# Optimization experiments

Measured on AMD Instinct MI355X. Metric: run time of the kernel, lower is better.

The kernel has to match this reference:

```python
import jax, jax.numpy as jnp
import numpy as np

B, T, E = 64, 64, 256
S, ENC = 128, 1024
RNN, ATT, DENSE = 1024, 1024, 8000


def setup_inputs() -> dict:
    key = jax.random.key(0)
    ks = jax.random.split(key, 16)
    s = 0.02
    return {
        "initial_input": jax.random.normal(ks[0], (B, T, E), jnp.float32),
        "hidden": jax.random.normal(ks[1], (B, RNN), jnp.float32),
        "cell": jax.random.normal(ks[2], (B, RNN), jnp.float32),
        "encoder_output": jax.random.normal(ks[3], (B, S, ENC), jnp.float32),
        "W1": jax.random.normal(ks[4], (RNN, ATT), jnp.float32) * s,
        "b1": jnp.zeros((ATT,), jnp.float32),
        "W2": jax.random.normal(ks[5], (ENC, ATT), jnp.float32) * s,
        "b2": jnp.zeros((ATT,), jnp.float32),
        "V": jax.random.normal(ks[6], (ATT, 1), jnp.float32) * s,
        "bV": jnp.zeros((1,), jnp.float32),
        "kernel": jax.random.normal(ks[7], (ENC + E, 4 * RNN), jnp.float32) * s,
        "rkernel": jax.random.normal(ks[8], (RNN, 4 * RNN), jnp.float32) * s,
        "bias": jnp.zeros((4 * RNN,), jnp.float32),
        "Wd": jax.random.normal(ks[9], (RNN, DENSE), jnp.float32) * s,
        "bd": jnp.zeros((DENSE,), jnp.float32),
        "seq_len": T,
    }


def _decode(initial_input, hidden, cell, encoder_output,
            W1, b1, W2, b2, V, bV, kernel, rkernel, bias, Wd, bd):
    # Keys W2(encoder_output) are step-independent: precompute once. [B,S,ATT]
    keys = jnp.einsum('bse,ea->bsa', encoder_output, W2) + b2

    def step(carry, x_t):
        h, c = carry
        # Bahdanau attention: score = V^T tanh(W1 h + W2 enc)
        q = h @ W1 + b1                                  # [B,ATT]
        score = jnp.tanh(q[:, None, :] + keys) @ V + bV   # [B,S,1]
        attn = jax.nn.softmax(score, axis=1)              # [B,S,1]
        ctx = jnp.sum(attn * encoder_output, axis=1)      # [B,ENC]
        # LSTM cell (Keras gate order i,f,g,o; sigmoid/tanh activations)
        inp = jnp.concatenate([ctx, x_t], axis=-1)        # [B,ENC+E]
        z = inp @ kernel + h @ rkernel + bias              # [B,4*RNN]
        i, f, g, o = jnp.split(z, 4, axis=-1)
        i = jax.nn.sigmoid(i)
        f = jax.nn.sigmoid(f)
        g = jnp.tanh(g)
        o = jax.nn.sigmoid(o)
        c_new = f * c + i * g
        h_new = o * jnp.tanh(c_new)
        logits = h_new @ Wd + bd                           # [B,DENSE]
        return (h_new, c_new), logits

    xs = jnp.swapaxes(initial_input, 0, 1)  # [T,B,E]
    (h, c), logits = jax.lax.scan(step, (hidden, cell), xs)
    outputs = jnp.swapaxes(logits, 0, 1)    # [B,T,DENSE]
    return outputs, h, c


def reference(initial_input, hidden, cell, encoder_output,
              W1, b1, W2, b2, V, bV, kernel, rkernel, bias, Wd, bd, seq_len):
    # seq_len == initial_input.shape[1] (static); the Python loop in the
    # original is expressed as an efficient lax.scan over decode steps.
    return _decode(initial_input[:, :seq_len, :], hidden, cell, encoder_output,
                   W1, b1, W2, b2, V, bV, kernel, rkernel, bias, Wd, bd)
```

## Files before the change

kernel.cpp:

```cpp
#include <hip/hip_runtime.h>
#include <hip/hip_bf16.h>
#include <stdint.h>


typedef __attribute__((ext_vector_type(8))) short short8;
typedef __attribute__((ext_vector_type(4))) float floatx4;
typedef __attribute__((ext_vector_type(4))) unsigned short ushortx4;

__device__ __forceinline__ float b2f(unsigned short u) {
    union { unsigned int i; float f; } v; v.i = ((unsigned int)u) << 16; return v.f;
}
__device__ __forceinline__ unsigned short f2b(float f) {
    union { float f; unsigned int i; } v; v.f = f;
    unsigned int r = v.i + 0x7fffu + ((v.i >> 16) & 1u);
    return (unsigned short)(r >> 16);
}
__device__ __forceinline__ float ftanh(float x) {
    x = fminf(15.f, fmaxf(-15.f, x));
    float e = __expf(2.f * x);
    return (e - 1.f) * __builtin_amdgcn_rcpf(e + 1.f);
}
__device__ __forceinline__ float vtanh(float x) {
    return __builtin_fmaf(-2.f, __builtin_amdgcn_rcpf(__expf(2.f * x) + 1.f), 1.f);
}
__device__ __forceinline__ float fsig(float x) {
    return __builtin_amdgcn_rcpf(1.f + __expf(-x));
}
__device__ __forceinline__ void ld_lds16(const void* g, void* l) {
    __builtin_amdgcn_global_load_lds((const __attribute__((address_space(1))) void*)g,
                                     (__attribute__((address_space(3))) void*)l, 16, 0, 0);
}

__device__ __forceinline__ void tr_tile(
    float (*tile)[33], const float* __restrict__ src, int srcld,
    unsigned short* __restrict__ dst, int dstld, int coloff, int perm,
    int bx, int by, int tid)
{
    const int k0 = by * 32, n0 = bx * 32;
    const int r = tid >> 3, c = (tid & 7) * 4;
    int n = n0 + c;
    int cn = perm ? ((((n >> 4) & 3) << 10) | ((n >> 6) << 4) | (n & 15)) : n;
    float4 v = *(const float4*)&src[(size_t)(k0 + r) * srcld + cn];
    tile[r][c + 0] = v.x; tile[r][c + 1] = v.y;
    tile[r][c + 2] = v.z; tile[r][c + 3] = v.w;
    __syncthreads();
    const int nr = tid >> 3, kc = (tid & 7) * 4;
    ushortx4 o;
    o[0] = f2b(tile[kc + 0][nr]);
    o[1] = f2b(tile[kc + 1][nr]);
    o[2] = f2b(tile[kc + 2][nr]);
    o[3] = f2b(tile[kc + 3][nr]);
    *(ushortx4*)&dst[(size_t)(n0 + nr) * dstld + coloff + k0 + kc] = o;
}

__global__ __launch_bounds__(256) void prep_all(
    const float* __restrict__ W2, unsigned short* __restrict__ W2T,
    const float* __restrict__ W1, unsigned short* __restrict__ W1T,
    const float* __restrict__ Wk, const float* __restrict__ rk,
    unsigned short* __restrict__ KRT,
    const float* __restrict__ Wd, unsigned short* __restrict__ WdT,
    const float* __restrict__ enc, unsigned short* __restrict__ enc_bf,
    const float* __restrict__ hidden, const float* __restrict__ cell,
    float* __restrict__ cb, unsigned short* __restrict__ hbf)
{
    __shared__ float tile[32][33];
    const int lid = blockIdx.x, tid = threadIdx.x;
    if (lid < 1024) {
        tr_tile(tile, W2, 1024, W2T, 1024, 0, 0, lid & 31, lid >> 5, tid);
    } else if (lid < 2048) {
        int l = lid - 1024;
        tr_tile(tile, W1, 1024, W1T, 1024, 0, 0, l & 31, l >> 5, tid);
    } else if (lid < 6144) {
        int l = lid - 2048;
        tr_tile(tile, Wk, 4096, KRT, 2304, 0, 1, l & 127, l >> 7, tid);
    } else if (lid < 7168) {
        int l = lid - 6144;
        tr_tile(tile, Wk + 1024 * 4096, 4096, KRT, 2304, 1024, 1, l & 127, l >> 7, tid);
    } else if (lid < 11264) {
        int l = lid - 7168;
        tr_tile(tile, rk, 4096, KRT, 2304, 1280, 1, l & 127, l >> 7, tid);
    } else if (lid < 19264) {
        int l = lid - 11264;
        tr_tile(tile, Wd, 8000, WdT, 1024, 0, 0, l % 250, l / 250, tid);
    } else if (lid < 27456) {
        int i = (lid - 19264) * 256 + tid;
        float4 v = ((const float4*)enc)[i];
        ushortx4 o;
        o[0] = f2b(v.x); o[1] = f2b(v.y); o[2] = f2b(v.z); o[3] = f2b(v.w);
        ((ushortx4*)enc_bf)[i] = o;
    } else {
        int idx = (lid - 27456) * 256 + tid;
        float h = hidden[idx], c = cell[idx];
        cb[idx] = c; hbf[idx] = f2b(h);
    }
}

__global__ __launch_bounds__(256) void gemm_bf16_128(
    const unsigned short* __restrict__ A, int lda,
    const unsigned short* __restrict__ BT, int ldbt, int K,
    float* __restrict__ Cf, unsigned short* __restrict__ Cb,
    int ldc, int ncols, const float* __restrict__ bias, int swz)
{
    __shared__ __align__(16) unsigned short As[128 * 32];
    __shared__ __align__(16) unsigned short Bs[128 * 32];
    const int tid = threadIdx.x, wave = tid >> 6, lane = tid & 63;
    const int q = lane >> 4, lm = lane & 15;
    const int wr = wave >> 1, wc = wave & 1;
    int bx = blockIdx.x, by = blockIdx.y;
    if (swz) {
        int bid = by * gridDim.x + bx;
        int xcd = bid & 7, l = bid >> 3;
        bx = xcd * 8 + (l & 7);
        by = l >> 3;
    }
    const int m0 = by * 128, n0 = bx * 128;
    const int srow = lane >> 2;
    const int gch = (lane & 3) ^ ((lane >> 3) & 3);
    const unsigned short* Ag0 = A + (size_t)(m0 + wave * 32 + srow) * lda + gch * 8;
    const unsigned short* Ag1 = Ag0 + (size_t)16 * lda;
    const unsigned short* Bg0 = BT + (size_t)(n0 + wave * 32 + srow) * ldbt + gch * 8;
    const unsigned short* Bg1 = Bg0 + (size_t)16 * ldbt;
    unsigned short* Al0 = &As[(wave * 32) * 32];
    unsigned short* Al1 = &As[(wave * 32 + 16) * 32];
    unsigned short* Bl0 = &Bs[(wave * 32) * 32];
    unsigned short* Bl1 = &Bs[(wave * 32 + 16) * 32];

    const floatx4 z4 = {0.f, 0.f, 0.f, 0.f};
    floatx4 acc[4][4];
#pragma unroll
    for (int i = 0; i < 4; i++)
#pragma unroll
        for (int j = 0; j < 4; j++) acc[i][j] = z4;
    const int ach = ((q ^ ((lm >> 1) & 3))) * 8;

    for (int kb = 0; kb < K; kb += 32) {
        ld_lds16(Ag0 + kb, Al0);
        ld_lds16(Ag1 + kb, Al1);
        ld_lds16(Bg0 + kb, Bl0);
        ld_lds16(Bg1 + kb, Bl1);
        __syncthreads();
        short8 a[4], b[4];
#pragma unroll
        for (int i = 0; i < 4; i++) a[i] = *(const short8*)&As[(wr * 64 + i * 16 + lm) * 32 + ach];
#pragma unroll
        for (int j = 0; j < 4; j++) b[j] = *(const short8*)&Bs[(wc * 64 + j * 16 + lm) * 32 + ach];
#pragma unroll
        for (int i = 0; i < 4; i++)
#pragma unroll
            for (int j = 0; j < 4; j++)
                acc[i][j] = __builtin_amdgcn_mfma_f32_16x16x32_bf16(a[i], b[j], acc[i][j], 0, 0, 0);
        __syncthreads();
    }
    const int rb = m0 + wr * 64 + q * 4;
#pragma unroll
    for (int i = 0; i < 4; i++) {
#pragma unroll
        for (int j = 0; j < 4; j++) {
            int col = n0 + wc * 64 + j * 16 + lm;
            if (col < ncols) {
                float bv = bias ? bias[col] : 0.f;
#pragma unroll
                for (int r = 0; r < 4; r++) {
                    float v = acc[i][j][r] + bv;
                    size_t idx = (size_t)(rb + i * 16 + r) * ldc + col;
                    if (Cf) Cf[idx] = v;
                    if (Cb) Cb[idx] = f2b(v);
                }
            }
        }
    }
}

__global__ __launch_bounds__(256) void gemm64_split(
    const unsigned short* __restrict__ A, int lda,
    const unsigned short* __restrict__ BT, int ldbt,
    int kchunk, float* __restrict__ Cpart, int ldc)
{
    __shared__ __align__(16) unsigned short As[4][64 * 32];
    __shared__ __align__(16) unsigned short Bs[4][64 * 32];
    const int tid = threadIdx.x, wave = tid >> 6, lane = tid & 63;
    const int q = lane >> 4, lm = lane & 15;
    const int n0 = blockIdx.x * 64;
    const int k0 = blockIdx.z * kchunk;
    const int srow = lane >> 2;
    const int gch = (lane & 3) ^ ((lane >> 3) & 3);
    const unsigned short* Ag = A + (size_t)(wave * 16 + srow) * lda + k0 + gch * 8;
    const unsigned short* Bg = BT + (size_t)(n0 + wave * 16 + srow) * ldbt + k0 + gch * 8;
    const int loff = (wave * 16) * 32;
    const floatx4 z4 = {0.f, 0.f, 0.f, 0.f};
    floatx4 acc0 = z4, acc1 = z4, acc2 = z4, acc3 = z4;
    const int ach = ((q ^ ((lm >> 1) & 3))) * 8;
    const int nit = kchunk >> 5;

#pragma unroll
    for (int p = 0; p < 3; ++p) {
        if (p < nit) {
            ld_lds16(Ag + p * 32, &As[p][loff]);
            ld_lds16(Bg + p * 32, &Bs[p][loff]);
        }
    }
    for (int it = 0; it < nit; ++it) {
        const int st = it & 3;
        if (it + 2 < nit)      asm volatile("s_waitcnt vmcnt(4)\n\ts_barrier" ::: "memory");
        else if (it + 1 < nit) asm volatile("s_waitcnt vmcnt(2)\n\ts_barrier" ::: "memory");
        else                   asm volatile("s_waitcnt vmcnt(0)\n\ts_barrier" ::: "memory");
        if (it + 3 < nit) {
            const int sn = (it + 3) & 3;
            ld_lds16(Ag + (it + 3) * 32, &As[sn][loff]);
            ld_lds16(Bg + (it + 3) * 32, &Bs[sn][loff]);
        }
        short8 a  = *(const short8*)&As[st][(wave * 16 + lm) * 32 + ach];
        short8 b0 = *(const short8*)&Bs[st][(0 * 16 + lm) * 32 + ach];
        short8 b1 = *(const short8*)&Bs[st][(1 * 16 + lm) * 32 + ach];
        short8 b2 = *(const short8*)&Bs[st][(2 * 16 + lm) * 32 + ach];
        short8 b3 = *(const short8*)&Bs[st][(3 * 16 + lm) * 32 + ach];
        acc0 = __builtin_amdgcn_mfma_f32_16x16x32_bf16(a, b0, acc0, 0, 0, 0);
        acc1 = __builtin_amdgcn_mfma_f32_16x16x32_bf16(a, b1, acc1, 0, 0, 0);
        acc2 = __builtin_amdgcn_mfma_f32_16x16x32_bf16(a, b2, acc2, 0, 0, 0);
        acc3 = __builtin_amdgcn_mfma_f32_16x16x32_bf16(a, b3, acc3, 0, 0, 0);
    }
    float* Cp = Cpart + (size_t)blockIdx.z * 64 * ldc;
    const int rb = wave * 16 + q * 4;
    floatx4 accs[4] = {acc0, acc1, acc2, acc3};
#pragma unroll
    for (int i = 0; i < 4; i++) {
        int col = n0 + i * 16 + lm;
#pragma unroll
        for (int r = 0; r < 4; r++) Cp[(size_t)(rb + r) * ldc + col] = accs[i][r];
    }
}

__global__ __launch_bounds__(256) void attn_scores(
    const float* __restrict__ qp, const float* __restrict__ b1,
    const unsigned short* __restrict__ keys,
    const float* __restrict__ V, const float* __restrict__ bV,
    float* __restrict__ sc)
{
    __shared__ float qs[1024];
    __shared__ float vs[1024];
    const int b = blockIdx.y, sg = blockIdx.x;
    const int tid = threadIdx.x, wave = tid >> 6, lane = tid & 63;
    {
        float4 a0 = ((const float4*)(qp + (size_t)b * 1024))[tid];
        float4 a1 = ((const float4*)(qp + 65536 + (size_t)b * 1024))[tid];
        float4 a2 = ((const float4*)(qp + 131072 + (size_t)b * 1024))[tid];
        float4 a3 = ((const float4*)(qp + 196608 + (size_t)b * 1024))[tid];
        float4 ab = ((const float4*)b1)[tid];
        float4 av = ((const float4*)V)[tid];
        float4 r;
        r.x = a0.x + a1.x + a2.x + a3.x + ab.x;
        r.y = a0.y + a1.y + a2.y + a3.y + ab.y;
        r.z = a0.z + a1.z + a2.z + a3.z + ab.z;
        r.w = a0.w + a1.w + a2.w + a3.w + ab.w;
        *(float4*)&qs[tid * 4] = r;
        *(float4*)&vs[tid * 4] = av;
    }
    __syncthreads();
    float qr[16], vr[16];
#pragma unroll
    for (int i = 0; i < 4; i++) {
        float4 tq = *(const float4*)&qs[lane * 16 + i * 4];
        float4 tv = *(const float4*)&vs[lane * 16 + i * 4];
        qr[i * 4 + 0] = tq.x; qr[i * 4 + 1] = tq.y; qr[i * 4 + 2] = tq.z; qr[i * 4 + 3] = tq.w;
        vr[i * 4 + 0] = tv.x; vr[i * 4 + 1] = tv.y; vr[i * 4 + 2] = tv.z; vr[i * 4 + 3] = tv.w;
    }
    const float bv0 = bV[0];
#pragma unroll
    for (int i = 0; i < 4; i++) {
        const int s = sg * 16 + wave * 4 + i;
        const uint4* kp = (const uint4*)(keys + ((size_t)(b * 128 + s)) * 1024 + lane * 16);
        uint4 k0 = kp[0], k1 = kp[1];
        float kf[16];
        kf[0] = b2f((unsigned short)(k0.x & 0xffff)); kf[1] = b2f((unsigned short)(k0.x >> 16));
        kf[2] = b2f((unsigned short)(k0.y & 0xffff)); kf[3] = b2f((unsigned short)(k0.y >> 16));
        kf[4] = b2f((unsigned short)(k0.z & 0xffff)); kf[5] = b2f((unsigned short)(k0.z >> 16));
        kf[6] = b2f((unsigned short)(k0.w & 0xffff)); kf[7] = b2f((unsigned short)(k0.w >> 16));
        kf[8] = b2f((unsigned short)(k1.x & 0xffff)); kf[9] = b2f((unsigned short)(k1.x >> 16));
        kf[10] = b2f((unsigned short)(k1.y & 0xffff)); kf[11] = b2f((unsigned short)(k1.y >> 16));
        kf[12] = b2f((unsigned short)(k1.z & 0xffff)); kf[13] = b2f((unsigned short)(k1.z >> 16));
        kf[14] = b2f((unsigned short)(k1.w & 0xffff)); kf[15] = b2f((unsigned short)(k1.w >> 16));
        float part = 0.f;
#pragma unroll
        for (int j = 0; j < 16; j++) part += vr[j] * vtanh(qr[j] + kf[j]);
#pragma unroll
        for (int off = 32; off; off >>= 1) part += __shfl_xor(part, off);
        if (lane == 0) sc[b * 128 + s] = part + bv0;
    }
}

__global__ __launch_bounds__(256) void softmax_ctx(
    const float* __restrict__ sc, const unsigned short* __restrict__ enc_bf,
    const float* __restrict__ x, const unsigned short* __restrict__ hbf,
    unsigned short* __restrict__ Axc, int t)
{
    __shared__ float attnv[128];
    __shared__ float red[4][64][2];
    __shared__ float smax_s, ssum_s;
    const int b = blockIdx.y, chunk = blockIdx.x;
    const int tid = threadIdx.x, wave = tid >> 6, lane = tid & 63;
    float sv = 0.f;
    if (tid < 128) { sv = sc[b * 128 + tid]; attnv[tid] = sv; }
    __syncthreads();
    if (tid < 64) {
        float m = fmaxf(attnv[tid], attnv[tid + 64]);
#pragma unroll
        for (int off = 32; off; off >>= 1) m = fmaxf(m, __shfl_xor(m, off));
        if (tid == 0) smax_s = m;
    }
    __syncthreads();
    if (tid < 128) attnv[tid] = __expf(sv - smax_s);
    __syncthreads();
    if (tid < 64) {
        float s2 = attnv[tid] + attnv[tid + 64];
#pragma unroll
        for (int off = 32; off; off >>= 1) s2 += __shfl_xor(s2, off);
        if (tid == 0) ssum_s = s2;
    }
    if (chunk < 2 && tid < 64) {
        int c2 = chunk * 128 + tid * 2;
        float x0 = x[((size_t)b * 64 + t) * 256 + c2];
        float x1 = x[((size_t)b * 64 + t) * 256 + c2 + 1];
        *(unsigned int*)&Axc[b * 2304 + 1024 + c2] =
            (unsigned int)f2b(x0) | ((unsigned int)f2b(x1) << 16);
    }
    if (tid < 64) {
        int c2 = chunk * 128 + tid * 2;
        *(unsigned int*)&Axc[b * 2304 + 1280 + c2] =
            *(const unsigned int*)&hbf[b * 1024 + c2];
    }
    const unsigned int* ep = (const unsigned int*)enc_bf + (size_t)b * 65536 + chunk * 64 + lane;
    __syncthreads();
    float ax = 0.f, ay = 0.f;
#pragma unroll 8
    for (int i = 0; i < 32; i++) {
        int s = wave * 32 + i;
        float a = attnv[s];
        unsigned int u = ep[(size_t)s * 512];
        ax += a * b2f((unsigned short)(u & 0xffff));
        ay += a * b2f((unsigned short)(u >> 16));
    }
    red[wave][lane][0] = ax; red[wave][lane][1] = ay;
    __syncthreads();
    if (tid < 64) {
        float rs = __builtin_amdgcn_rcpf(ssum_s);
        float fx = (red[0][lane][0] + red[1][lane][0] + red[2][lane][0] + red[3][lane][0]) * rs;
        float fy = (red[0][lane][1] + red[1][lane][1] + red[2][lane][1] + red[3][lane][1]) * rs;
        *(unsigned int*)&Axc[b * 2304 + chunk * 128 + lane * 2] =
            (unsigned int)f2b(fx) | ((unsigned int)f2b(fy) << 16);
    }
}

__global__ __launch_bounds__(512) void gemm_gates(
    const unsigned short* __restrict__ Axc,
    const unsigned short* __restrict__ KRT,
    const float* __restrict__ bz,
    float* __restrict__ cb,
    unsigned short* __restrict__ hbf, unsigned short* __restrict__ Hall, int t,
    float* __restrict__ out, int last)
{
    __shared__ __align__(16) char smem[65536];
    unsigned short* As = (unsigned short*)smem;
    unsigned short* Bs = (unsigned short*)(smem + 32768);
    float* red = (float*)smem;
    const int tid = threadIdx.x, wave = tid >> 6, lane = tid & 63;
    const int q = lane >> 4, lm = lane & 15;
    const int h = wave >> 2, wm = wave & 3;
    const int bx = blockIdx.x;
    const int srow = lane >> 2;
    const int gch = (lane & 3) ^ ((lane >> 3) & 3);
    const unsigned short* Ag = Axc + (size_t)(wm * 16 + srow) * 2304 + h * 1152 + gch * 8;
    const unsigned short* Bg = KRT + (size_t)(bx * 64 + wm * 16 + srow) * 2304 + h * 1152 + gch * 8;
    const int tileoff = h * 2048;
    const int ldoff = tileoff + (wm * 16) * 32;
    const floatx4 z4 = {0.f, 0.f, 0.f, 0.f};
    floatx4 acc0 = z4, acc1 = z4, acc2 = z4, acc3 = z4;
    const int ach = ((q ^ ((lm >> 1) & 3))) * 8;

#pragma unroll
    for (int p = 0; p < 3; ++p) {
        ld_lds16(Ag + p * 32, &As[p * 4096 + ldoff]);
        ld_lds16(Bg + p * 32, &Bs[p * 4096 + ldoff]);
    }
    for (int it = 0; it < 36; ++it) {
        const int st = it & 3;
        if (it < 34)       asm volatile("s_waitcnt vmcnt(4)\n\ts_barrier" ::: "memory");
        else if (it == 34) asm volatile("s_waitcnt vmcnt(2)\n\ts_barrier" ::: "memory");
        else               asm volatile("s_waitcnt vmcnt(0)\n\ts_barrier" ::: "memory");
        if (it + 3 < 36) {
            const int sn = (it + 3) & 3;
            ld_lds16(Ag + (it + 3) * 32, &As[sn * 4096 + ldoff]);
            ld_lds16(Bg + (it + 3) * 32, &Bs[sn * 4096 + ldoff]);
        }
        const unsigned short* Ast = &As[st * 4096 + tileoff];
        const unsigned short* Bst = &Bs[st * 4096 + tileoff];
        short8 a  = *(const short8*)&Ast[(wm * 16 + lm) * 32 + ach];
        short8 b0 = *(const short8*)&Bst[(0 * 16 + lm) * 32 + ach];
        short8 b1 = *(const short8*)&Bst[(1 * 16 + lm) * 32 + ach];
        short8 b2 = *(const short8*)&Bst[(2 * 16 + lm) * 32 + ach];
        short8 b3 = *(const short8*)&Bst[(3 * 16 + lm) * 32 + ach];
        acc0 = __builtin_amdgcn_mfma_f32_16x16x32_bf16(a, b0, acc0, 0, 0, 0);
        acc1 = __builtin_amdgcn_mfma_f32_16x16x32_bf16(a, b1, acc1, 0, 0, 0);
        acc2 = __builtin_amdgcn_mfma_f32_16x16x32_bf16(a, b2, acc2, 0, 0, 0);
        acc3 = __builtin_amdgcn_mfma_f32_16x16x32_bf16(a, b3, acc3, 0, 0, 0);
    }
    __syncthreads();
    if (h == 1) {
        float* rp = &red[(wm * 64 + lane) * 16];
        *(floatx4*)&rp[0]  = acc0; *(floatx4*)&rp[4]  = acc1;
        *(floatx4*)&rp[8]  = acc2; *(floatx4*)&rp[12] = acc3;
    }
    __syncthreads();
    if (h == 0) {
        const float* rp = &red[(wm * 64 + lane) * 16];
        acc0 += *(const floatx4*)&rp[0];
        acc1 += *(const floatx4*)&rp[4];
        acc2 += *(const floatx4*)&rp[8];
        acc3 += *(const floatx4*)&rp[12];
        const int col = bx * 16 + lm;
        const float bzi = bz[col], bzf = bz[1024 + col];
        const float bzg = bz[2048 + col], bzo = bz[3072 + col];
#pragma unroll
        for (int r = 0; r < 4; ++r) {
            const int b = wm * 16 + q * 4 + r;
            float zi = acc0[r] + bzi;
            float zf = acc1[r] + bzf;
            float zg = acc2[r] + bzg;
            float zo = acc3[r] + bzo;
            float ii = fsig(zi), ff = fsig(zf), gg = ftanh(zg), oo = fsig(zo);
            const int idx = b * 1024 + col;
            float cn = ff * cb[idx] + ii * gg;
            float hn = oo * ftanh(cn);
            cb[idx] = cn;
            unsigned short hb = f2b(hn);
            hbf[idx] = hb;
            Hall[((size_t)b * 64 + t) * 1024 + col] = hb;
            if (last) {
                out[32768000 + idx] = hn;
                out[32768000 + 65536 + idx] = cn;
            }
        }
    }
}

extern "C" void kernel_launch(void* const* d_in, const int* in_sizes, int n_in,
                              void* d_out, int out_size, void* d_ws, size_t ws_size,
                              hipStream_t stream)
{
    const float* x      = (const float*)d_in[0];
    const float* hidden = (const float*)d_in[1];
    const float* cell   = (const float*)d_in[2];
    const float* enc    = (const float*)d_in[3];
    const float* W1     = (const float*)d_in[4];
    const float* b1     = (const float*)d_in[5];
    const float* W2     = (const float*)d_in[6];
    const float* b2     = (const float*)d_in[7];
    const float* V      = (const float*)d_in[8];
    const float* bV     = (const float*)d_in[9];
    const float* Wk     = (const float*)d_in[10];
    const float* rk     = (const float*)d_in[11];
    const float* bz     = (const float*)d_in[12];
    const float* Wd     = (const float*)d_in[13];
    const float* bd     = (const float*)d_in[14];
    float* out = (float*)d_out;

    char* ws = (char*)d_ws;
    unsigned short* enc_bf  = (unsigned short*)(ws + 0);
    unsigned short* keys_bf = (unsigned short*)(ws + 16777216);
    unsigned short* W1T     = (unsigned short*)(ws + 33554432);
    unsigned short* KRT     = (unsigned short*)(ws + 35651584);
    unsigned short* WdT     = (unsigned short*)(ws + 54525952);
    unsigned short* Hall    = (unsigned short*)(ws + 71303168);
    unsigned short* W2T     = Hall;
    unsigned short* Axc     = (unsigned short*)(ws + 79691776);
    float* qp    = (float*)(ws + 79986688);
    unsigned short* hbf     = (unsigned short*)(ws + 81035264);
    float* scbuf = (float*)(ws + 81166336);
    float* cb    = (float*)(ws + 81199104);

    prep_all<<<27712, 256, 0, stream>>>(W2, W2T, W1, W1T, Wk, rk, KRT, Wd, WdT,
                                        enc, enc_bf, hidden, cell, cb, hbf);

    gemm_bf16_128<<<dim3(8, 64), 256, 0, stream>>>(enc_bf, 1024, W2T, 1024, 1024,
                                                   nullptr, keys_bf, 1024, 1024, b2, 0);

    for (int t = 0; t < 64; t++) {
        gemm64_split<<<dim3(16, 1, 4), 256, 0, stream>>>(hbf, 1024, W1T, 1024, 256, qp, 1024);
        attn_scores<<<dim3(8, 64), 256, 0, stream>>>(qp, b1, keys_bf, V, bV, scbuf);
        softmax_ctx<<<dim3(8, 64), 256, 0, stream>>>(scbuf, enc_bf, x, hbf, Axc, t);
        gemm_gates<<<64, 512, 0, stream>>>(Axc, KRT, bz, cb, hbf, Hall, t,
                                           out, (t == 63) ? 1 : 0);
    }

    gemm_bf16_128<<<dim3(64, 32), 256, 0, stream>>>(Hall, 1024, WdT, 1024, 1024,
                                                    out, nullptr, 8000, 8000, bd, 1);
}
```

Baseline: 2.344 ms.

## Fuse query GEMM, attention scores and softmax-context into one kernel with atomic flags

```diff
diff --git a/kernel.cpp b/kernel.cpp
--- a/kernel.cpp
+++ b/kernel.cpp
@@ -61,7 +61,8 @@
     const float* __restrict__ Wd, unsigned short* __restrict__ WdT,
     const float* __restrict__ enc, unsigned short* __restrict__ enc_bf,
     const float* __restrict__ hidden, const float* __restrict__ cell,
-    float* __restrict__ cb, unsigned short* __restrict__ hbf)
+    float* __restrict__ cb, unsigned short* __restrict__ hbf,
+    unsigned int* __restrict__ zt)
 {
     __shared__ float tile[32][33];
     const int lid = blockIdx.x, tid = threadIdx.x;
@@ -88,10 +89,13 @@
         ushortx4 o;
         o[0] = f2b(v.x); o[1] = f2b(v.y); o[2] = f2b(v.z); o[3] = f2b(v.w);
         ((ushortx4*)enc_bf)[i] = o;
-    } else {
+    } else if (lid < 27712) {
         int idx = (lid - 27456) * 256 + tid;
         float h = hidden[idx], c = cell[idx];
         cb[idx] = c; hbf[idx] = f2b(h);
+    } else {
+        int i = (lid - 27712) * 256 + tid;
+        if (i < 8256) zt[i] = 0u;
     }
 }
 
@@ -171,89 +175,115 @@
     }
 }
 
-__global__ __launch_bounds__(256) void gemm64_split(
-    const unsigned short* __restrict__ A, int lda,
-    const unsigned short* __restrict__ BT, int ldbt,
-    int kchunk, float* __restrict__ Cpart, int ldc)
-{
-    __shared__ __align__(16) unsigned short As[4][64 * 32];
-    __shared__ __align__(16) unsigned short Bs[4][64 * 32];
-    const int tid = threadIdx.x, wave = tid >> 6, lane = tid & 63;
-    const int q = lane >> 4, lm = lane & 15;
-    const int n0 = blockIdx.x * 64;
-    const int k0 = blockIdx.z * kchunk;
-    const int srow = lane >> 2;
-    const int gch = (lane & 3) ^ ((lane >> 3) & 3);
-    const unsigned short* Ag = A + (size_t)(wave * 16 + srow) * lda + k0 + gch * 8;
-    const unsigned short* Bg = BT + (size_t)(n0 + wave * 16 + srow) * ldbt + k0 + gch * 8;
-    const int loff = (wave * 16) * 32;
-    const floatx4 z4 = {0.f, 0.f, 0.f, 0.f};
-    floatx4 acc0 = z4, acc1 = z4, acc2 = z4, acc3 = z4;
-    const int ach = ((q ^ ((lm >> 1) & 3))) * 8;
-    const int nit = kchunk >> 5;
-
-#pragma unroll
-    for (int p = 0; p < 3; ++p) {
-        if (p < nit) {
-            ld_lds16(Ag + p * 32, &As[p][loff]);
-            ld_lds16(Bg + p * 32, &Bs[p][loff]);
-        }
-    }
-    for (int it = 0; it < nit; ++it) {
-        const int st = it & 3;
-        if (it + 2 < nit)      asm volatile("s_waitcnt vmcnt(4)\n\ts_barrier" ::: "memory");
-        else if (it + 1 < nit) asm volatile("s_waitcnt vmcnt(2)\n\ts_barrier" ::: "memory");
-        else                   asm volatile("s_waitcnt vmcnt(0)\n\ts_barrier" ::: "memory");
-        if (it + 3 < nit) {
-            const int sn = (it + 3) & 3;
-            ld_lds16(Ag + (it + 3) * 32, &As[sn][loff]);
-            ld_lds16(Bg + (it + 3) * 32, &Bs[sn][loff]);
-        }
-        short8 a  = *(const short8*)&As[st][(wave * 16 + lm) * 32 + ach];
-        short8 b0 = *(const short8*)&Bs[st][(0 * 16 + lm) * 32 + ach];
-        short8 b1 = *(const short8*)&Bs[st][(1 * 16 + lm) * 32 + ach];
-        short8 b2 = *(const short8*)&Bs[st][(2 * 16 + lm) * 32 + ach];
-        short8 b3 = *(const short8*)&Bs[st][(3 * 16 + lm) * 32 + ach];
-        acc0 = __builtin_amdgcn_mfma_f32_16x16x32_bf16(a, b0, acc0, 0, 0, 0);
-        acc1 = __builtin_amdgcn_mfma_f32_16x16x32_bf16(a, b1, acc1, 0, 0, 0);
-        acc2 = __builtin_amdgcn_mfma_f32_16x16x32_bf16(a, b2, acc2, 0, 0, 0);
-        acc3 = __builtin_amdgcn_mfma_f32_16x16x32_bf16(a, b3, acc3, 0, 0, 0);
-    }
-    float* Cp = Cpart + (size_t)blockIdx.z * 64 * ldc;
-    const int rb = wave * 16 + q * 4;
-    floatx4 accs[4] = {acc0, acc1, acc2, acc3};
-#pragma unroll
-    for (int i = 0; i < 4; i++) {
-        int col = n0 + i * 16 + lm;
-#pragma unroll
-        for (int r = 0; r < 4; r++) Cp[(size_t)(rb + r) * ldc + col] = accs[i][r];
-    }
-}
-
-__global__ __launch_bounds__(256) void attn_scores(
-    const float* __restrict__ qp, const float* __restrict__ b1,
+__global__ __launch_bounds__(256) void qattn_k(
+    const unsigned short* __restrict__ hbf, const unsigned short* __restrict__ W1T,
+    float* __restrict__ qp, const float* __restrict__ b1,
     const unsigned short* __restrict__ keys,
     const float* __restrict__ V, const float* __restrict__ bV,
-    float* __restrict__ sc)
+    const unsigned short* __restrict__ enc_bf, const float* __restrict__ x,
+    unsigned short* __restrict__ Axc,
+    float* __restrict__ esbuf, float* __restrict__ den,
+    unsigned int* __restrict__ qcnt, unsigned int* __restrict__ scnt, int t)
 {
-    __shared__ float qs[1024];
-    __shared__ float vs[1024];
-    const int b = blockIdx.y, sg = blockIdx.x;
-    const int tid = threadIdx.x, wave = tid >> 6, lane = tid & 63;
+    __shared__ __align__(16) char smem[33024];
+    const int blk = blockIdx.x, tid = threadIdx.x;
+    const int wave = tid >> 6, lane = tid & 63;
+    const floatx4 z4 = {0.f, 0.f, 0.f, 0.f};
+
+    if (blk < 64) {
+        unsigned short* As = (unsigned short*)smem;
+        unsigned short* Bs = (unsigned short*)(smem + 16384);
+        const int q = lane >> 4, lm = lane & 15;
+        const int bx = blk & 15, kz = blk >> 4;
+        const int n0 = bx * 64, k0 = kz * 256;
+        const int srow = lane >> 2;
+        const int gch = (lane & 3) ^ ((lane >> 3) & 3);
+        const unsigned short* Ag = hbf + (size_t)(wave * 16 + srow) * 1024 + k0 + gch * 8;
+        const unsigned short* Bg = W1T + (size_t)(n0 + wave * 16 + srow) * 1024 + k0 + gch * 8;
+        const int loff = (wave * 16) * 32;
+        floatx4 acc0 = z4, acc1 = z4, acc2 = z4, acc3 = z4;
+        const int ach = ((q ^ ((lm >> 1) & 3))) * 8;
+#pragma unroll
+        for (int p = 0; p < 3; ++p) {
+            ld_lds16(Ag + p * 32, &As[p * 2048 + loff]);
+            ld_lds16(Bg + p * 32, &Bs[p * 2048 + loff]);
+        }
+#pragma unroll 1
+        for (int it = 0; it < 8; ++it) {
+            const int st = it & 3;
+            if (it < 6)       asm volatile("s_waitcnt vmcnt(4)\n\ts_barrier" ::: "memory");
+            else if (it == 6) asm volatile("s_waitcnt vmcnt(2)\n\ts_barrier" ::: "memory");
+            else              asm volatile("s_waitcnt vmcnt(0)\n\ts_barrier" ::: "memory");
+            if (it + 3 < 8) {
+                const int sn = (it + 3) & 3;
+                ld_lds16(Ag + (it + 3) * 32, &As[sn * 2048 + loff]);
+                ld_lds16(Bg + (it + 3) * 32, &Bs[sn * 2048 + loff]);
+            }
+            short8 a  = *(const short8*)&As[st * 2048 + (wave * 16 + lm) * 32 + ach];
+            short8 b0 = *(const short8*)&Bs[st * 2048 + (0 * 16 + lm) * 32 + ach];
+            short8 b1v = *(const short8*)&Bs[st * 2048 + (1 * 16 + lm) * 32 + ach];
+            short8 b2 = *(const short8*)&Bs[st * 2048 + (2 * 16 + lm) * 32 + ach];
+            short8 b3 = *(const short8*)&Bs[st * 2048 + (3 * 16 + lm) * 32 + ach];
+            acc0 = __builtin_amdgcn_mfma_f32_16x16x32_bf16(a, b0, acc0, 0, 0, 0);
+            acc1 = __builtin_amdgcn_mfma_f32_16x16x32_bf16(a, b1v, acc1, 0, 0, 0);
+            acc2 = __builtin_amdgcn_mfma_f32_16x16x32_bf16(a, b2, acc2, 0, 0, 0);
+            acc3 = __builtin_amdgcn_mfma_f32_16x16x32_bf16(a, b3, acc3, 0, 0, 0);
+        }
+        float* Cp = qp + (size_t)kz * 65536;
+        const int rb = wave * 16 + q * 4;
+        floatx4 accs[4] = {acc0, acc1, acc2, acc3};
+#pragma unroll
+        for (int i = 0; i < 4; i++) {
+            int col = n0 + i * 16 + lm;
+#pragma unroll
+            for (int r = 0; r < 4; r++) Cp[(size_t)(rb + r) * 1024 + col] = accs[i][r];
+        }
+        __syncthreads();
+        if (tid == 0) {
+            __threadfence();
+            __hip_atomic_fetch_add(&qcnt[t], 1u, __ATOMIC_RELEASE, __HIP_MEMORY_SCOPE_AGENT);
+        }
+        return;
+    }
+
+    const int ab = blk - 64;
+    const int sg = ab & 7, b = ab >> 3;
+    float* qs    = (float*)smem;
+    float* vs    = (float*)(smem + 4096);
+    float* attnv = (float*)(smem + 8192);
+    float* redc  = (float*)(smem + 8704);
+    float* misc  = (float*)(smem + 10752);
+
+    if (sg == 0 && tid < 128) {
+        float x0 = x[((size_t)b * 64 + t) * 256 + tid * 2];
+        float x1 = x[((size_t)b * 64 + t) * 256 + tid * 2 + 1];
+        ((unsigned int*)&Axc[b * 2304 + 1024])[tid] =
+            (unsigned int)f2b(x0) | ((unsigned int)f2b(x1) << 16);
+    }
+    if (tid < 64) {
+        int c2 = sg * 128 + tid * 2;
+        *(unsigned int*)&Axc[b * 2304 + 1280 + c2] =
+            *(const unsigned int*)&hbf[b * 1024 + c2];
+    }
     {
-        float4 a0 = ((const float4*)(qp + (size_t)b * 1024))[tid];
-        float4 a1 = ((const float4*)(qp + 65536 + (size_t)b * 1024))[tid];
-        float4 a2 = ((const float4*)(qp + 131072 + (size_t)b * 1024))[tid];
-        float4 a3 = ((const float4*)(qp + 196608 + (size_t)b * 1024))[tid];
-        float4 ab = ((const float4*)b1)[tid];
         float4 av = ((const float4*)V)[tid];
-        float4 r;
-        r.x = a0.x + a1.x + a2.x + a3.x + ab.x;
-        r.y = a0.y + a1.y + a2.y + a3.y + ab.y;
-        r.z = a0.z + a1.z + a2.z + a3.z + ab.z;
-        r.w = a0.w + a1.w + a2.w + a3.w + ab.w;
+        float4 ab1 = ((const float4*)b1)[tid];
+        *(float4*)&vs[tid * 4] = av;
+        *(float4*)&qs[tid * 4] = ab1;
+    }
+    if (tid == 0) {
+        while (__hip_atomic_load(&qcnt[t], __ATOMIC_ACQUIRE, __HIP_MEMORY_SCOPE_AGENT) < 64u)
+            __builtin_amdgcn_s_sleep(2);
+    }
+    __syncthreads();
+    {
+        float4 r = *(float4*)&qs[tid * 4];
+#pragma unroll
+        for (int p = 0; p < 4; ++p) {
+            float4 a = ((const float4*)(qp + (size_t)p * 65536 + (size_t)b * 1024))[tid];
+            r.x += a.x; r.y += a.y; r.z += a.z; r.w += a.w;
+        }
         *(float4*)&qs[tid * 4] = r;
-        *(float4*)&vs[tid * 4] = av;
     }
     __syncthreads();
     float qr[16], vr[16];
@@ -265,6 +295,7 @@
         vr[i * 4 + 0] = tv.x; vr[i * 4 + 1] = tv.y; vr[i * 4 + 2] = tv.z; vr[i * 4 + 3] = tv.w;
     }
     const float bv0 = bV[0];
+    float* es16 = misc + 8;
 #pragma unroll
     for (int i = 0; i < 4; i++) {
         const int s = sg * 16 + wave * 4 + i;
@@ -284,51 +315,27 @@
         for (int j = 0; j < 16; j++) part += vr[j] * vtanh(qr[j] + kf[j]);
 #pragma unroll
         for (int off = 32; off; off >>= 1) part += __shfl_xor(part, off);
-        if (lane == 0) sc[b * 128 + s] = part + bv0;
-    }
-}
-
-__global__ __launch_bounds__(256) void softmax_ctx(
-    const float* __restrict__ sc, const unsigned short* __restrict__ enc_bf,
-    const float* __restrict__ x, const unsigned short* __restrict__ hbf,
-    unsigned short* __restrict__ Axc, int t)
-{
-    __shared__ float attnv[128];
-    __shared__ float red[4][64][2];
-    __shared__ float smax_s, ssum_s;
-    const int b = blockIdx.y, chunk = blockIdx.x;
-    const int tid = threadIdx.x, wave = tid >> 6, lane = tid & 63;
-    float sv = 0.f;
-    if (tid < 128) { sv = sc[b * 128 + tid]; attnv[tid] = sv; }
-    __syncthreads();
-    if (tid < 64) {
-        float m = fmaxf(attnv[tid], attnv[tid + 64]);
-#pragma unroll
-        for (int off = 32; off; off >>= 1) m = fmaxf(m, __shfl_xor(m, off));
-        if (tid == 0) smax_s = m;
-    }
-    __syncthreads();
-    if (tid < 128) attnv[tid] = __expf(sv - smax_s);
-    __syncthreads();
-    if (tid < 64) {
-        float s2 = attnv[tid] + attnv[tid + 64];
-#pragma unroll
-        for (int off = 32; off; off >>= 1) s2 += __shfl_xor(s2, off);
-        if (tid == 0) ssum_s = s2;
-    }
-    if (chunk < 2 && tid < 64) {
-        int c2 = chunk * 128 + tid * 2;
-        float x0 = x[((size_t)b * 64 + t) * 256 + c2];
-        float x1 = x[((size_t)b * 64 + t) * 256 + c2 + 1];
-        *(unsigned int*)&Axc[b * 2304 + 1024 + c2] =
-            (unsigned int)f2b(x0) | ((unsigned int)f2b(x1) << 16);
-    }
-    if (tid < 64) {
-        int c2 = chunk * 128 + tid * 2;
-        *(unsigned int*)&Axc[b * 2304 + 1280 + c2] =
-            *(const unsigned int*)&hbf[b * 1024 + c2];
-    }
-    const unsigned int* ep = (const unsigned int*)enc_bf + (size_t)b * 65536 + chunk * 64 + lane;
+        if (lane == 0) es16[wave * 4 + i] = __expf(part + bv0);
+    }
+    __syncthreads();
+    if (tid == 0) {
+        float d = 0.f;
+#pragma unroll
+        for (int k = 0; k < 16; k++) d += es16[k];
+        atomicAdd(&den[t * 64 + b], d);
+    }
+    if (tid < 16) esbuf[b * 128 + sg * 16 + tid] = es16[tid];
+    __syncthreads();
+    if (tid == 0) {
+        __threadfence();
+        __hip_atomic_fetch_add(&scnt[t * 64 + b], 1u, __ATOMIC_RELEASE, __HIP_MEMORY_SCOPE_AGENT);
+        while (__hip_atomic_load(&scnt[t * 64 + b], __ATOMIC_ACQUIRE, __HIP_MEMORY_SCOPE_AGENT) < 8u)
+            __builtin_amdgcn_s_sleep(2);
+        misc[0] = __hip_atomic_load(&den[t * 64 + b], __ATOMIC_RELAXED, __HIP_MEMORY_SCOPE_AGENT);
+    }
+    __syncthreads();
+    if (tid < 128) attnv[tid] = esbuf[b * 128 + tid];
+    const unsigned int* ep = (const unsigned int*)enc_bf + (size_t)b * 65536 + sg * 64 + lane;
     __syncthreads();
     float ax = 0.f, ay = 0.f;
 #pragma unroll 8
@@ -339,13 +346,15 @@
         ax += a * b2f((unsigned short)(u & 0xffff));
         ay += a * b2f((unsigned short)(u >> 16));
     }
-    red[wave][lane][0] = ax; red[wave][lane][1] = ay;
+    redc[(wave * 64 + lane) * 2] = ax; redc[(wave * 64 + lane) * 2 + 1] = ay;
     __syncthreads();
     if (tid < 64) {
-        float rs = __builtin_amdgcn_rcpf(ssum_s);
-        float fx = (red[0][lane][0] + red[1][lane][0] + red[2][lane][0] + red[3][lane][0]) * rs;
-        float fy = (red[0][lane][1] + red[1][lane][1] + red[2][lane][1] + red[3][lane][1]) * rs;
-        *(unsigned int*)&Axc[b * 2304 + chunk * 128 + lane * 2] =
+        float rs = __builtin_amdgcn_rcpf(misc[0]);
+        float fx = (redc[lane * 2] + redc[(64 + lane) * 2] +
+                    redc[(128 + lane) * 2] + redc[(192 + lane) * 2]) * rs;
+        float fy = (redc[lane * 2 + 1] + redc[(64 + lane) * 2 + 1] +
+                    redc[(128 + lane) * 2 + 1] + redc[(192 + lane) * 2 + 1]) * rs;
+        *(unsigned int*)&Axc[b * 2304 + sg * 128 + lane * 2] =
             (unsigned int)f2b(fx) | ((unsigned int)f2b(fy) << 16);
     }
 }
@@ -474,19 +483,21 @@
     unsigned short* Axc     = (unsigned short*)(ws + 79691776);
     float* qp    = (float*)(ws + 79986688);
     unsigned short* hbf     = (unsigned short*)(ws + 81035264);
-    float* scbuf = (float*)(ws + 81166336);
+    float* esbuf = (float*)(ws + 81166336);
     float* cb    = (float*)(ws + 81199104);
-
-    prep_all<<<27712, 256, 0, stream>>>(W2, W2T, W1, W1T, Wk, rk, KRT, Wd, WdT,
-                                        enc, enc_bf, hidden, cell, cb, hbf);
+    unsigned int* qcnt = (unsigned int*)(ws + 81461248);
+    unsigned int* scnt = qcnt + 64;
+    float*        den  = (float*)(scnt + 4096);
+
+    prep_all<<<27745, 256, 0, stream>>>(W2, W2T, W1, W1T, Wk, rk, KRT, Wd, WdT,
+                                        enc, enc_bf, hidden, cell, cb, hbf, qcnt);
 
     gemm_bf16_128<<<dim3(8, 64), 256, 0, stream>>>(enc_bf, 1024, W2T, 1024, 1024,
                                                    nullptr, keys_bf, 1024, 1024, b2, 0);
 
     for (int t = 0; t < 64; t++) {
-        gemm64_split<<<dim3(16, 1, 4), 256, 0, stream>>>(hbf, 1024, W1T, 1024, 256, qp, 1024);
-        attn_scores<<<dim3(8, 64), 256, 0, stream>>>(qp, b1, keys_bf, V, bV, scbuf);
-        softmax_ctx<<<dim3(8, 64), 256, 0, stream>>>(scbuf, enc_bf, x, hbf, Axc, t);
+        qattn_k<<<576, 256, 0, stream>>>(hbf, W1T, qp, b1, keys_bf, V, bV,
+                                         enc_bf, x, Axc, esbuf, den, qcnt, scnt, t);
         gemm_gates<<<64, 512, 0, stream>>>(Axc, KRT, bz, cb, hbf, Hall, t,
                                            out, (t == 63) ? 1 : 0);
     }
```

Measured after the change: 5.870 ms. +150.4%, slower.

## Double-buffer LSTM input buffer, drop softmax max pass, swizzle keys GEMM

Applied to the files above, without the earlier changes.

```diff
diff --git a/kernel.cpp b/kernel.cpp
--- a/kernel.cpp
+++ b/kernel.cpp
@@ -61,7 +61,9 @@
     const float* __restrict__ Wd, unsigned short* __restrict__ WdT,
     const float* __restrict__ enc, unsigned short* __restrict__ enc_bf,
     const float* __restrict__ hidden, const float* __restrict__ cell,
-    float* __restrict__ cb, unsigned short* __restrict__ hbf)
+    const float* __restrict__ x,
+    float* __restrict__ cb, unsigned short* __restrict__ hbf,
+    unsigned short* __restrict__ Axc0)
 {
     __shared__ float tile[32][33];
     const int lid = blockIdx.x, tid = threadIdx.x;
@@ -88,10 +90,20 @@
         ushortx4 o;
         o[0] = f2b(v.x); o[1] = f2b(v.y); o[2] = f2b(v.z); o[3] = f2b(v.w);
         ((ushortx4*)enc_bf)[i] = o;
-    } else {
+    } else if (lid < 27712) {
         int idx = (lid - 27456) * 256 + tid;
         float h = hidden[idx], c = cell[idx];
-        cb[idx] = c; hbf[idx] = f2b(h);
+        cb[idx] = c;
+        unsigned short hb = f2b(h);
+        hbf[idx] = hb;
+        Axc0[(idx >> 10) * 2304 + 1280 + (idx & 1023)] = hb;
+    } else {
+        int p = (lid - 27712) * 256 + tid;
+        int b = p >> 7, e2 = (p & 127) * 2;
+        float x0 = x[((size_t)b * 64) * 256 + e2];
+        float x1 = x[((size_t)b * 64) * 256 + e2 + 1];
+        *(unsigned int*)&Axc0[b * 2304 + 1024 + e2] =
+            (unsigned int)f2b(x0) | ((unsigned int)f2b(x1) << 16);
     }
 }
 
@@ -107,11 +119,16 @@
     const int q = lane >> 4, lm = lane & 15;
     const int wr = wave >> 1, wc = wave & 1;
     int bx = blockIdx.x, by = blockIdx.y;
-    if (swz) {
+    if (swz == 1) {
         int bid = by * gridDim.x + bx;
         int xcd = bid & 7, l = bid >> 3;
         bx = xcd * 8 + (l & 7);
         by = l >> 3;
+    } else if (swz == 2) {
+        int bid = by * gridDim.x + bx;
+        int xcd = bid & 7, m = bid >> 3;
+        by = xcd * 8 + (m & 7);
+        bx = m >> 3;
     }
     const int m0 = by * 128, n0 = bx * 128;
     const int srow = lane >> 2;
@@ -290,43 +307,20 @@
 
 __global__ __launch_bounds__(256) void softmax_ctx(
     const float* __restrict__ sc, const unsigned short* __restrict__ enc_bf,
-    const float* __restrict__ x, const unsigned short* __restrict__ hbf,
-    unsigned short* __restrict__ Axc, int t)
+    unsigned short* __restrict__ Axc_t)
 {
     __shared__ float attnv[128];
     __shared__ float red[4][64][2];
-    __shared__ float smax_s, ssum_s;
+    __shared__ float ssum_s;
     const int b = blockIdx.y, chunk = blockIdx.x;
     const int tid = threadIdx.x, wave = tid >> 6, lane = tid & 63;
-    float sv = 0.f;
-    if (tid < 128) { sv = sc[b * 128 + tid]; attnv[tid] = sv; }
-    __syncthreads();
-    if (tid < 64) {
-        float m = fmaxf(attnv[tid], attnv[tid + 64]);
-#pragma unroll
-        for (int off = 32; off; off >>= 1) m = fmaxf(m, __shfl_xor(m, off));
-        if (tid == 0) smax_s = m;
-    }
-    __syncthreads();
-    if (tid < 128) attnv[tid] = __expf(sv - smax_s);
+    if (tid < 128) attnv[tid] = __expf(sc[b * 128 + tid]);
     __syncthreads();
     if (tid < 64) {
         float s2 = attnv[tid] + attnv[tid + 64];
 #pragma unroll
         for (int off = 32; off; off >>= 1) s2 += __shfl_xor(s2, off);
         if (tid == 0) ssum_s = s2;
-    }
-    if (chunk < 2 && tid < 64) {
-        int c2 = chunk * 128 + tid * 2;
-        float x0 = x[((size_t)b * 64 + t) * 256 + c2];
-        float x1 = x[((size_t)b * 64 + t) * 256 + c2 + 1];
-        *(unsigned int*)&Axc[b * 2304 + 1024 + c2] =
-            (unsigned int)f2b(x0) | ((unsigned int)f2b(x1) << 16);
-    }
-    if (tid < 64) {
-        int c2 = chunk * 128 + tid * 2;
-        *(unsigned int*)&Axc[b * 2304 + 1280 + c2] =
-            *(const unsigned int*)&hbf[b * 1024 + c2];
     }
     const unsigned int* ep = (const unsigned int*)enc_bf + (size_t)b * 65536 + chunk * 64 + lane;
     __syncthreads();
@@ -345,17 +339,19 @@
         float rs = __builtin_amdgcn_rcpf(ssum_s);
         float fx = (red[0][lane][0] + red[1][lane][0] + red[2][lane][0] + red[3][lane][0]) * rs;
         float fy = (red[0][lane][1] + red[1][lane][1] + red[2][lane][1] + red[3][lane][1]) * rs;
-        *(unsigned int*)&Axc[b * 2304 + chunk * 128 + lane * 2] =
+        *(unsigned int*)&Axc_t[b * 2304 + chunk * 128 + lane * 2] =
             (unsigned int)f2b(fx) | ((unsigned int)f2b(fy) << 16);
     }
 }
 
 __global__ __launch_bounds__(512) void gemm_gates(
-    const unsigned short* __restrict__ Axc,
+    const unsigned short* __restrict__ Axc_r,
+    unsigned short* __restrict__ Axc_w,
     const unsigned short* __restrict__ KRT,
     const float* __restrict__ bz,
     float* __restrict__ cb,
-    unsigned short* __restrict__ hbf, unsigned short* __restrict__ Hall, int t,
+    unsigned short* __restrict__ hbf, unsigned short* __restrict__ Hall,
+    const float* __restrict__ x, int t,
     float* __restrict__ out, int last)
 {
     __shared__ __align__(16) char smem[65536];
@@ -368,7 +364,7 @@
     const int bx = blockIdx.x;
     const int srow = lane >> 2;
     const int gch = (lane & 3) ^ ((lane >> 3) & 3);
-    const unsigned short* Ag = Axc + (size_t)(wm * 16 + srow) * 2304 + h * 1152 + gch * 8;
+    const unsigned short* Ag = Axc_r + (size_t)(wm * 16 + srow) * 2304 + h * 1152 + gch * 8;
     const unsigned short* Bg = KRT + (size_t)(bx * 64 + wm * 16 + srow) * 2304 + h * 1152 + gch * 8;
     const int tileoff = h * 2048;
     const int ldoff = tileoff + (wm * 16) * 32;
@@ -408,6 +404,15 @@
         float* rp = &red[(wm * 64 + lane) * 16];
         *(floatx4*)&rp[0]  = acc0; *(floatx4*)&rp[4]  = acc1;
         *(floatx4*)&rp[8]  = acc2; *(floatx4*)&rp[12] = acc3;
+        if (t < 63) {
+            int local = tid - 256;
+            if (local < 128) {
+                const float* xp = x + ((size_t)bx * 64 + t + 1) * 256 + local * 2;
+                float x0 = xp[0], x1 = xp[1];
+                ((unsigned int*)&Axc_w[bx * 2304 + 1024])[local] =
+                    (unsigned int)f2b(x0) | ((unsigned int)f2b(x1) << 16);
+            }
+        }
     }
     __syncthreads();
     if (h == 0) {
@@ -434,6 +439,7 @@
             unsigned short hb = f2b(hn);
             hbf[idx] = hb;
             Hall[((size_t)b * 64 + t) * 1024 + col] = hb;
+            if (t < 63) Axc_w[b * 2304 + 1280 + col] = hb;
             if (last) {
                 out[32768000 + idx] = hn;
                 out[32768000 + 65536 + idx] = cn;
@@ -472,23 +478,25 @@
     unsigned short* Hall    = (unsigned short*)(ws + 71303168);
     unsigned short* W2T     = Hall;
     unsigned short* Axc     = (unsigned short*)(ws + 79691776);
-    float* qp    = (float*)(ws + 79986688);
-    unsigned short* hbf     = (unsigned short*)(ws + 81035264);
-    float* scbuf = (float*)(ws + 81166336);
-    float* cb    = (float*)(ws + 81199104);
-
-    prep_all<<<27712, 256, 0, stream>>>(W2, W2T, W1, W1T, Wk, rk, KRT, Wd, WdT,
-                                        enc, enc_bf, hidden, cell, cb, hbf);
+    float* qp    = (float*)(ws + 80281600);
+    unsigned short* hbf     = (unsigned short*)(ws + 81330176);
+    float* scbuf = (float*)(ws + 81461248);
+    float* cb    = (float*)(ws + 81494016);
+
+    prep_all<<<27744, 256, 0, stream>>>(W2, W2T, W1, W1T, Wk, rk, KRT, Wd, WdT,
+                                        enc, enc_bf, hidden, cell, x, cb, hbf, Axc);
 
     gemm_bf16_128<<<dim3(8, 64), 256, 0, stream>>>(enc_bf, 1024, W2T, 1024, 1024,
-                                                   nullptr, keys_bf, 1024, 1024, b2, 0);
+                                                   nullptr, keys_bf, 1024, 1024, b2, 2);
 
     for (int t = 0; t < 64; t++) {
+        unsigned short* Axc_r = Axc + (size_t)(t & 1) * 147456;
+        unsigned short* Axc_w = Axc + (size_t)((t + 1) & 1) * 147456;
         gemm64_split<<<dim3(16, 1, 4), 256, 0, stream>>>(hbf, 1024, W1T, 1024, 256, qp, 1024);
         attn_scores<<<dim3(8, 64), 256, 0, stream>>>(qp, b1, keys_bf, V, bV, scbuf);
-        softmax_ctx<<<dim3(8, 64), 256, 0, stream>>>(scbuf, enc_bf, x, hbf, Axc, t);
-        gemm_gates<<<64, 512, 0, stream>>>(Axc, KRT, bz, cb, hbf, Hall, t,
-                                           out, (t == 63) ? 1 : 0);
+        softmax_ctx<<<dim3(8, 64), 256, 0, stream>>>(scbuf, enc_bf, Axc_r);
+        gemm_gates<<<64, 512, 0, stream>>>(Axc_r, Axc_w, KRT, bz, cb, hbf, Hall,
+                                           x, t, out, (t == 63) ? 1 : 0);
     }
 
     gemm_bf16_128<<<dim3(64, 32), 256, 0, stream>>>(Hall, 1024, WdT, 1024, 1024,
```

Result: no change. 2.315 ms (-1.2%).
